# Optimization experiments

Hardware: AMD Instinct MI355X
Metric: run time of the kernel (lower is better)

The kernel has to match this reference:

```python
import jax, jax.numpy as jnp
import numpy as np

B, F, K = 8192, 128, 32  # batch, num_features, bins per feature (D = F*K = 4096)
T_TOTAL = 1000           # num_timesteps for the cosine schedule
EPS_LOG = 1e-8
EPS_GUMBEL = 1e-30


def _cosine_sigmas(T):
    # matches _make_schedule('cosine', T)
    steps = jnp.arange(T + 1, dtype=jnp.float32)
    alphas_cumprod = jnp.cos((steps / T + 0.008) / 1.008 * jnp.pi / 2) ** 2
    return 1.0 - alphas_cumprod[1:] / alphas_cumprod[:-1]  # [T]


def setup_inputs() -> dict:
    key = jax.random.key(0)
    k1, k2 = jax.random.split(key)
    # log one-hot x0, as built in mixed_loss: log(one_hot + 1e-8)
    x0 = jax.random.randint(k1, (B, F), 0, K)
    log_x0 = jnp.log(jax.nn.one_hot(x0, K, dtype=jnp.float32) + EPS_LOG).reshape(B, F * K)
    # uniform noise for the Gumbel-max trick (rand_like in the original)
    u = jax.random.uniform(k2, (B, F * K), dtype=jnp.float32)
    return {"log_x0": log_x0, "u": u, "t": 64}


def reference(log_x0, u, t):
    # q_sample: t sequential q_forward steps, fused over features via a scan.
    sigmas = _cosine_sigmas(T_TOTAL)[:t]          # [t], t is a static Python int
    Q = jnp.ones((K, K), jnp.float32) / K         # fixed uniform score matrix

    def step(log_p, sigma_t):
        p = jnp.exp(log_p)                                     # [B,F,K]
        p_next = (1.0 - sigma_t) * p + sigma_t * jnp.einsum('bfi,ij->bfj', p, Q)
        return jnp.log(p_next + EPS_LOG), None

    log_p0 = log_x0.reshape(B, F, K)
    log_p, _ = jax.lax.scan(step, log_p0, sigmas)              # [B,F,K]

    # log_sample_categorical: Gumbel-max per feature block
    g = -jnp.log(-jnp.log(u.reshape(B, F, K) + EPS_GUMBEL) + EPS_GUMBEL)
    sample = jnp.argmax(log_p + g, axis=-1)                    # [B,F]
    log_xt = jnp.log(jax.nn.one_hot(sample, K, dtype=jnp.float32) + EPS_LOG)
    return log_xt.reshape(B, F * K)
```

## Files before the change

### kernel.cpp

```cpp
#include <hip/hip_runtime.h>
#include <math.h>


__device__ __forceinline__ float cr_logf32(float x) { return (float)log((double)x); }

__device__ __forceinline__ float cr_g(float u) {
    float c0 = __fadd_rn(u, 1e-30f);
    float t2 = cr_logf32(c0);
    float t3 = __fadd_rn(-t2, 1e-30f);
    float t4 = cr_logf32(t3);
    return -t4;
}

__global__ void traj_kernel(const float* __restrict__ log_x0,
                            const int* __restrict__ t_ptr,
                            float* __restrict__ traj) {
    __shared__ float ac[1001];
    __shared__ float sig[1000];
    __shared__ float init2[2];
    int t = *t_ptr;
    if (t > 1000) t = 1000;
    if (t < 0) t = 0;

    for (int s = threadIdx.x; s <= t; s += blockDim.x) {
        float a = __fdiv_rn((float)s, 1000.0f);
        float b = __fadd_rn(a, 0.008f);
        float c = __fdiv_rn(b, 1.008f);
        float d = __fmul_rn(c, 0x1.921fb6p+1f);
        float e = __fmul_rn(d, 0.5f);
        float cs = (float)cos((double)e);
        ac[s] = __fmul_rn(cs, cs);
    }
    if (threadIdx.x == 0) {
        float hotf = -1e30f, coldf = 1e30f;
        for (int j = 0; j < 32; ++j) {
            float v = log_x0[j];
            hotf = fmaxf(hotf, v);
            coldf = fminf(coldf, v);
        }
        init2[0] = hotf;
        init2[1] = coldf;
        traj[64] = coldf;
        *(int*)(traj + 66) = 0;
    }
    __syncthreads();
    for (int s = threadIdx.x + 1; s <= t; s += blockDim.x)
        sig[s - 1] = __fsub_rn(1.0f, __fdiv_rn(ac[s], ac[s - 1]));
    __syncthreads();

    if (threadIdx.x < 32) {
        const int h = threadIdx.x;
        float lh = init2[0];
        float lc = init2[1];
        for (int k = 0; k < t; ++k) {
            float sg = sig[k];
            float ph = (float)exp((double)lh);
            float pc = (float)exp((double)lc);
            float th = __fmul_rn(ph, 0.03125f);
            float tc = __fmul_rn(pc, 0.03125f);
            float acc = 0.0f;
            for (int i = 0; i < 32; ++i)
                acc = __fadd_rn(acc, (i == h) ? th : tc);
            float s1  = __fsub_rn(1.0f, sg);
            float sm  = __fmul_rn(sg, acc);
            float phn = __fadd_rn(__fmul_rn(s1, ph), sm);
            float pcn = __fadd_rn(__fmul_rn(s1, pc), sm);
            lh = cr_logf32(__fadd_rn(phn, 1e-8f));
            lc = cr_logf32(__fadd_rn(pcn, 1e-8f));
        }
        traj[h]      = lh;
        traj[32 + h] = lc;
    }
}

__global__ void sample_kernel(const float4* __restrict__ log_x0,
                              const float4* __restrict__ u,
                              float* __restrict__ trajm,
                              float4* __restrict__ out,
                              int ntile, int cap) {
    __shared__ float lds_u[4][2112];
    __shared__ unsigned char lds_h[4][64];
    __shared__ float lh_s[32], lc_s[32];
    __shared__ float coldv_s;
    if (threadIdx.x < 32) {
        lh_s[threadIdx.x] = trajm[threadIdx.x];
        lc_s[threadIdx.x] = trajm[32 + threadIdx.x];
    }
    if (threadIdx.x == 0) coldv_s = trajm[64];
    __syncthreads();
    const float coldv = coldv_s;
    int* cnt  = (int*)(trajm + 66);
    int* list = cnt + 1;

    const int w     = threadIdx.x >> 6;
    const int lane  = threadIdx.x & 63;
    const int wid   = (int)((blockIdx.x * blockDim.x + threadIdx.x) >> 6);
    const int nwav  = (int)((gridDim.x * blockDim.x) >> 6);

    for (int tile = wid; tile < ntile; tile += nwav) {
        const size_t fb8 = (size_t)tile * 512;

        #pragma unroll
        for (int k = 0; k < 8; ++k) {
            const float4 v = u[fb8 + k * 64 + lane];
            const int lj = k * 64 + lane;
            const int fl = lj >> 3;
            const int q  = lj & 7;
            float* dst = &lds_u[w][fl * 33 + q * 4];
            dst[0] = v.x; dst[1] = v.y; dst[2] = v.z; dst[3] = v.w;
        }
        #pragma unroll
        for (int k = 0; k < 8; ++k) {
            const float4 xv = log_x0[fb8 + k * 64 + lane];
            int p = -1;
            p = (xv.x > -1.0f) ? 0 : p;
            p = (xv.y > -1.0f) ? 1 : p;
            p = (xv.z > -1.0f) ? 2 : p;
            p = (xv.w > -1.0f) ? 3 : p;
            const unsigned long long bal = __ballot(p >= 0);
            const int sgb = lane & ~7;
            const unsigned mm = (unsigned)((bal >> sgb) & 0xFFull);
            const int hlane = (int)__ffs(mm) - 1;
            const int psrc  = __shfl(p, sgb + ((hlane < 0) ? 0 : hlane), 64);
            const int hbin  = (hlane < 0) ? 255 : (hlane * 4 + psrc);
            if ((lane & 7) == 0)
                lds_h[w][k * 8 + (lane >> 3)] = (unsigned char)hbin;
        }
        __syncthreads();

        const int   h  = (int)lds_h[w][lane];
        const int   hc = (h > 31) ? 0 : h;
        const float lh = lh_s[hc];
        const float lc = lc_s[hc];
        const float* urow = &lds_u[w][lane * 33];

        float t1u = -1.0f, t2u = -1.0f; int t1i = 0;
        #pragma unroll
        for (int j = 0; j < 32; ++j) {
            const float cu = (j == hc) ? -1.0f : urow[j];
            const bool gt1 = cu > t1u;
            const bool gt2 = cu > t2u;
            t2u = gt1 ? t1u : (gt2 ? cu : t2u);
            t1i = gt1 ? j : t1i;
            t1u = gt1 ? cu : t1u;
        }
        const float uhot = urow[hc];

        const float s_hot  = __fadd_rn(lh, cr_g(uhot));
        const float s_cold = __fadd_rn(lc, cr_g(t1u));
        int widx;
        if (s_hot > s_cold)      widx = hc;
        else if (s_hot < s_cold) widx = t1i;
        else                     widx = (hc < t1i) ? hc : t1i;

        if (__builtin_expect(((t1u - t2u) < 1e-6f) | (h > 31), 0)) {
            int slot = atomicAdd(cnt, 1);
            if (slot < cap) list[slot] = tile * 64 + lane;
        }

        #pragma unroll
        for (int k = 0; k < 8; ++k) {
            const int src = k * 8 + (lane >> 3);
            const int wk  = __shfl(widx, src, 64);
            const int qb  = (lane & 7) * 4;
            float4 o;
            o.x = (wk == qb    ) ? 0.0f : coldv;
            o.y = (wk == qb + 1) ? 0.0f : coldv;
            o.z = (wk == qb + 2) ? 0.0f : coldv;
            o.w = (wk == qb + 3) ? 0.0f : coldv;
            out[fb8 + k * 64 + lane] = o;
        }
        __syncthreads();
    }
}

__global__ void fixup_kernel(const float* __restrict__ log_x0,
                             const float* __restrict__ u,
                             float* __restrict__ trajm,
                             float* __restrict__ out,
                             int cap) {
    __shared__ float lh_s[32], lc_s[32];
    __shared__ float coldv_s;
    if (threadIdx.x < 32) {
        lh_s[threadIdx.x] = trajm[threadIdx.x];
        lc_s[threadIdx.x] = trajm[32 + threadIdx.x];
    }
    if (threadIdx.x == 0) coldv_s = trajm[64];
    __syncthreads();
    const float coldv = coldv_s;
    const int* cnt  = (const int*)(trajm + 66);
    const int* list = cnt + 1;

    int n = *cnt;
    if (n > cap) n = cap;

    const int lane32  = threadIdx.x & 31;
    const int group   = (int)((blockIdx.x * blockDim.x + threadIdx.x) >> 5);
    const int ngroups = (int)((gridDim.x * blockDim.x) >> 5);
    const int shift   = (threadIdx.x & 32) ? 32 : 0;

    for (int i = group; i < n; i += ngroups) {
        const int f = list[i];
        const int base = f * 32 + lane32;
        const float uf = u[base];
        const float xf = log_x0[base];
        const bool hot = xf > -1.0f;

        unsigned long long bal = __ballot(hot);
        unsigned mm = (unsigned)(bal >> shift);
        int h = mm ? (__ffs(mm) - 1) : 0;

        float L = hot ? lh_s[h] : lc_s[h];
        float s = __fadd_rn(L, cr_g(uf));

        int idx = lane32;
        #pragma unroll
        for (int m = 16; m > 0; m >>= 1) {
            float os = __shfl_xor(s,   m, 32);
            int   oi = __shfl_xor(idx, m, 32);
            if (os > s || (os == s && oi < idx)) {
                s = os;
                idx = oi;
            }
        }
        out[base] = (lane32 == idx) ? 0.0f : coldv;
    }
}

extern "C" void kernel_launch(void* const* d_in, const int* in_sizes, int n_in,
                              void* d_out, int out_size, void* d_ws, size_t ws_size,
                              hipStream_t stream) {
    const float* log_x0 = (const float*)d_in[0];
    const float* u      = (const float*)d_in[1];
    const int*   t_ptr  = (const int*)d_in[2];
    float* out  = (float*)d_out;
    float* traj = (float*)d_ws;

    const int nfeat = in_sizes[0] / 32;
    const int ntile = nfeat / 64;

    long long avail = (long long)(ws_size / 4) - 80;
    int cap = (avail < 0) ? 0 : ((avail > 16384) ? 16384 : (int)avail);

    traj_kernel<<<1, 128, 0, stream>>>(log_x0, t_ptr, traj);

    sample_kernel<<<2048, 256, 0, stream>>>((const float4*)log_x0,
                                            (const float4*)u, traj,
                                            (float4*)out, ntile, cap);

    fixup_kernel<<<256, 256, 0, stream>>>(log_x0, u, traj, out, cap);
}
```

Before: 137.0 us.

## Issue all tile loads upfront, one tile per wave, float4 LDS with rotated reads

The sample kernel drops the grid-stride loop and launches exactly one 64-feature tile per wave, so the grid is sized to the data. All eight log_x0 and u float4 loads are issued into registers before any processing, to expose more memory-level parallelism. u is written to LDS as whole float4s without the 33-stride padding, and each lane reads its row as float4s starting at a lane-rotated offset to avoid bank conflicts. The risks are higher register pressure and relying on ntile being divisible by 4.

```diff
diff --git a/kernel.cpp b/kernel.cpp
--- a/kernel.cpp
+++ b/kernel.cpp
@@ -73,12 +73,22 @@
     }
 }
 
+#define SCANB(VAL, IDX)                                         \
+    {                                                           \
+        const float cu = ((IDX) == hc) ? -1.0f : (VAL);         \
+        const bool gt1 = cu > t1u;                              \
+        const bool gt2 = cu > t2u;                              \
+        t2u = gt1 ? t1u : (gt2 ? cu : t2u);                     \
+        t1i = gt1 ? (IDX) : t1i;                                \
+        t1u = gt1 ? cu : t1u;                                   \
+    }
+
 __global__ void sample_kernel(const float4* __restrict__ log_x0,
                               const float4* __restrict__ u,
                               float* __restrict__ trajm,
                               float4* __restrict__ out,
-                              int ntile, int cap) {
-    __shared__ float lds_u[4][2112];
+                              int cap) {
+    __shared__ float lds_u[4][2048];
     __shared__ unsigned char lds_h[4][64];
     __shared__ float lh_s[32], lc_s[32];
     __shared__ float coldv_s;
@@ -87,90 +97,85 @@
         lc_s[threadIdx.x] = trajm[32 + threadIdx.x];
     }
     if (threadIdx.x == 0) coldv_s = trajm[64];
-    __syncthreads();
-    const float coldv = coldv_s;
     int* cnt  = (int*)(trajm + 66);
     int* list = cnt + 1;
 
-    const int w     = threadIdx.x >> 6;
-    const int lane  = threadIdx.x & 63;
-    const int wid   = (int)((blockIdx.x * blockDim.x + threadIdx.x) >> 6);
-    const int nwav  = (int)((gridDim.x * blockDim.x) >> 6);
-
-    for (int tile = wid; tile < ntile; tile += nwav) {
-        const size_t fb8 = (size_t)tile * 512;
-
-        #pragma unroll
-        for (int k = 0; k < 8; ++k) {
-            const float4 v = u[fb8 + k * 64 + lane];
-            const int lj = k * 64 + lane;
-            const int fl = lj >> 3;
-            const int q  = lj & 7;
-            float* dst = &lds_u[w][fl * 33 + q * 4];
-            dst[0] = v.x; dst[1] = v.y; dst[2] = v.z; dst[3] = v.w;
-        }
-        #pragma unroll
-        for (int k = 0; k < 8; ++k) {
-            const float4 xv = log_x0[fb8 + k * 64 + lane];
-            int p = -1;
-            p = (xv.x > -1.0f) ? 0 : p;
-            p = (xv.y > -1.0f) ? 1 : p;
-            p = (xv.z > -1.0f) ? 2 : p;
-            p = (xv.w > -1.0f) ? 3 : p;
-            const unsigned long long bal = __ballot(p >= 0);
-            const int sgb = lane & ~7;
-            const unsigned mm = (unsigned)((bal >> sgb) & 0xFFull);
-            const int hlane = (int)__ffs(mm) - 1;
-            const int psrc  = __shfl(p, sgb + ((hlane < 0) ? 0 : hlane), 64);
-            const int hbin  = (hlane < 0) ? 255 : (hlane * 4 + psrc);
-            if ((lane & 7) == 0)
-                lds_h[w][k * 8 + (lane >> 3)] = (unsigned char)hbin;
-        }
-        __syncthreads();
-
-        const int   h  = (int)lds_h[w][lane];
-        const int   hc = (h > 31) ? 0 : h;
-        const float lh = lh_s[hc];
-        const float lc = lc_s[hc];
-        const float* urow = &lds_u[w][lane * 33];
-
-        float t1u = -1.0f, t2u = -1.0f; int t1i = 0;
-        #pragma unroll
-        for (int j = 0; j < 32; ++j) {
-            const float cu = (j == hc) ? -1.0f : urow[j];
-            const bool gt1 = cu > t1u;
-            const bool gt2 = cu > t2u;
-            t2u = gt1 ? t1u : (gt2 ? cu : t2u);
-            t1i = gt1 ? j : t1i;
-            t1u = gt1 ? cu : t1u;
-        }
-        const float uhot = urow[hc];
-
-        const float s_hot  = __fadd_rn(lh, cr_g(uhot));
-        const float s_cold = __fadd_rn(lc, cr_g(t1u));
-        int widx;
-        if (s_hot > s_cold)      widx = hc;
-        else if (s_hot < s_cold) widx = t1i;
-        else                     widx = (hc < t1i) ? hc : t1i;
-
-        if (__builtin_expect(((t1u - t2u) < 1e-6f) | (h > 31), 0)) {
-            int slot = atomicAdd(cnt, 1);
-            if (slot < cap) list[slot] = tile * 64 + lane;
-        }
-
-        #pragma unroll
-        for (int k = 0; k < 8; ++k) {
-            const int src = k * 8 + (lane >> 3);
-            const int wk  = __shfl(widx, src, 64);
-            const int qb  = (lane & 7) * 4;
-            float4 o;
-            o.x = (wk == qb    ) ? 0.0f : coldv;
-            o.y = (wk == qb + 1) ? 0.0f : coldv;
-            o.z = (wk == qb + 2) ? 0.0f : coldv;
-            o.w = (wk == qb + 3) ? 0.0f : coldv;
-            out[fb8 + k * 64 + lane] = o;
-        }
-        __syncthreads();
+    const int w    = threadIdx.x >> 6;
+    const int lane = threadIdx.x & 63;
+    const int tile = (int)((blockIdx.x * blockDim.x + threadIdx.x) >> 6);
+    const size_t fb4 = (size_t)tile * 512;
+
+    float4 xr[8];
+    #pragma unroll
+    for (int k = 0; k < 8; ++k) xr[k] = log_x0[fb4 + k * 64 + lane];
+    float4 ur[8];
+    #pragma unroll
+    for (int k = 0; k < 8; ++k) ur[k] = u[fb4 + k * 64 + lane];
+
+    const int sgb = lane & ~7;
+    #pragma unroll
+    for (int k = 0; k < 8; ++k) {
+        const float4 xv = xr[k];
+        int p = -1;
+        p = (xv.x > -1.0f) ? 0 : p;
+        p = (xv.y > -1.0f) ? 1 : p;
+        p = (xv.z > -1.0f) ? 2 : p;
+        p = (xv.w > -1.0f) ? 3 : p;
+        const unsigned long long bal = __ballot(p >= 0);
+        const unsigned mm = (unsigned)((bal >> sgb) & 0xFFull);
+        const int hlane = (int)__ffs(mm) - 1;
+        const int psrc  = __shfl(p, sgb + ((hlane < 0) ? 0 : hlane), 64);
+        const int hbin  = (hlane < 0) ? 255 : (hlane * 4 + psrc);
+        if ((lane & 7) == 0)
+            lds_h[w][k * 8 + (lane >> 3)] = (unsigned char)hbin;
+    }
+
+    #pragma unroll
+    for (int k = 0; k < 8; ++k)
+        *(float4*)&lds_u[w][k * 256 + lane * 4] = ur[k];
+
+    __syncthreads();
+
+    const int   h  = (int)lds_h[w][lane];
+    const int   hc = (h > 31) ? 0 : h;
+    const float lh = lh_s[hc];
+    const float lc = lc_s[hc];
+    const float coldv = coldv_s;
+    const float4* urow4 = (const float4*)&lds_u[w][lane * 32];
+
+    float t1u = -1.0f, t2u = -1.0f; int t1i = 0;
+    #pragma unroll
+    for (int q = 0; q < 8; ++q) {
+        const int qq = (q + lane) & 7;
+        const float4 v = urow4[qq];
+        const int b0 = qq * 4;
+        SCANB(v.x, b0) SCANB(v.y, b0 + 1) SCANB(v.z, b0 + 2) SCANB(v.w, b0 + 3)
+    }
+    const float uhot = lds_u[w][lane * 32 + hc];
+
+    const float s_hot  = __fadd_rn(lh, cr_g(uhot));
+    const float s_cold = __fadd_rn(lc, cr_g(t1u));
+    int widx;
+    if (s_hot > s_cold)      widx = hc;
+    else if (s_hot < s_cold) widx = t1i;
+    else                     widx = (hc < t1i) ? hc : t1i;
+
+    if (__builtin_expect(((t1u - t2u) < 1e-6f) | (h > 31), 0)) {
+        int slot = atomicAdd(cnt, 1);
+        if (slot < cap) list[slot] = tile * 64 + lane;
+    }
+
+    #pragma unroll
+    for (int k = 0; k < 8; ++k) {
+        const int src = k * 8 + (lane >> 3);
+        const int wk  = __shfl(widx, src, 64);
+        const int qb  = (lane & 7) * 4;
+        float4 o;
+        o.x = (wk == qb    ) ? 0.0f : coldv;
+        o.y = (wk == qb + 1) ? 0.0f : coldv;
+        o.z = (wk == qb + 2) ? 0.0f : coldv;
+        o.w = (wk == qb + 3) ? 0.0f : coldv;
+        out[fb4 + k * 64 + lane] = o;
     }
 }
 
@@ -238,15 +243,16 @@
 
     const int nfeat = in_sizes[0] / 32;
     const int ntile = nfeat / 64;
+    const int nblk  = ntile / 4;
 
     long long avail = (long long)(ws_size / 4) - 80;
     int cap = (avail < 0) ? 0 : ((avail > 16384) ? 16384 : (int)avail);
 
     traj_kernel<<<1, 128, 0, stream>>>(log_x0, t_ptr, traj);
 
-    sample_kernel<<<2048, 256, 0, stream>>>((const float4*)log_x0,
+    sample_kernel<<<nblk, 256, 0, stream>>>((const float4*)log_x0,
                                             (const float4*)u, traj,
-                                            (float4*)out, ntile, cap);
+                                            (float4*)out, cap);
 
     fixup_kernel<<<256, 256, 0, stream>>>(log_x0, u, traj, out, cap);
 }
```

Result: slower. 140.3 us (+2.4%).
